# Kernel tuning notes

Hardware: AMD Instinct MI355X
Metric: run time of the kernel (lower is better)

## Reference

```python
import jax, jax.numpy as jnp
import numpy as np
import math

HIDDEN = 2048
HEADS = 16
HEAD_DIM = HIDDEN // HEADS
MAX_SEQ = 4096
ROPE_BASE = 10000.0


def rope_cos_sin(seq_len):
    # (seq_len, head_dim//2) angle table
    inv_freq = 1.0 / (ROPE_BASE ** (jnp.arange(0, HEAD_DIM, 2, dtype=jnp.float32) / HEAD_DIM))
    t = jnp.arange(seq_len, dtype=jnp.float32)
    ang = jnp.einsum('s,f->sf', t, inv_freq)
    return jnp.cos(ang), jnp.sin(ang)


def apply_rope(x, cos, sin):
    # x: (b, s, h, d); interleaved complex pairs along last dim
    b, s, h, d = x.shape
    xr = x.reshape(b, s, h, d // 2, 2)
    x0, x1 = xr[..., 0], xr[..., 1]
    c = cos[:s][None, :, None, :]
    sn = sin[:s][None, :, None, :]
    o0 = x0 * c - x1 * sn
    o1 = x0 * sn + x1 * c
    return jnp.stack([o0, o1], axis=-1).reshape(b, s, h, d)


def setup_inputs() -> dict:
    key = jax.random.key(0)
    k1, k2, k3, k4, k5, k6 = jax.random.split(key, 6)
    B, SQ, SK = 2, 2048, 2048
    x = jax.random.normal(k1, (B, SQ, HIDDEN), dtype=jnp.float32)
    enc = jax.random.normal(k2, (B, SK, HIDDEN), dtype=jnp.float32)
    mask = jnp.ones((B, SK), dtype=jnp.int32)
    scale = 0.02
    Wq = jax.random.normal(k3, (HIDDEN, HIDDEN), dtype=jnp.float32) * scale
    Wk = jax.random.normal(k4, (HIDDEN, HIDDEN), dtype=jnp.float32) * scale
    Wv = jax.random.normal(k5, (HIDDEN, HIDDEN), dtype=jnp.float32) * scale
    Wo = jax.random.normal(k6, (HIDDEN, HIDDEN), dtype=jnp.float32) * scale
    return {"x": x, "encoder_output": enc, "encoder_attention_mask": mask,
            "Wq": Wq, "Wk": Wk, "Wv": Wv, "Wo": Wo}


def reference(x, encoder_output, encoder_attention_mask, Wq, Wk, Wv, Wo):
    B, SQ, _ = x.shape
    SK = encoder_output.shape[1]
    # nn.Linear(bias=False): y = x @ W^T
    q = (x @ Wq.T).reshape(B, SQ, HEADS, HEAD_DIM)
    k = (encoder_output @ Wk.T).reshape(B, SK, HEADS, HEAD_DIM)
    v = (encoder_output @ Wv.T).reshape(B, SK, HEADS, HEAD_DIM)
    cos, sin = rope_cos_sin(max(SQ, SK))
    q = apply_rope(q, cos, sin)
    k = apply_rope(k, cos, sin)
    scale = math.sqrt(HEAD_DIM)
    # (b, h, sq, sk) scores
    scores = jnp.einsum('bqhd,bkhd->bhqk', q, k) / scale
    mask = encoder_attention_mask[:, None, None, :]
    scores = jnp.where(mask == 0, -jnp.inf, scores)
    attn = jax.nn.softmax(scores, axis=-1)
    out = jnp.einsum('bhqk,bkhd->bqhd', attn, v).reshape(B, SQ, HIDDEN)
    return out @ Wo.T
```

## Files before the change

kernel.cpp:

```cpp
#include <hip/hip_runtime.h>
#include <stdint.h>


#define LOG2E 1.44269504088896340736f
#define INV2PI 0.15915494309189535f

typedef __attribute__((ext_vector_type(8))) short bf16x8;
typedef __attribute__((ext_vector_type(8))) uint16_t u16x8;
typedef __attribute__((ext_vector_type(4))) uint16_t u16x4;
typedef __attribute__((ext_vector_type(4))) float f32x4;

__device__ __forceinline__ uint16_t f2bf(float f) {
  union { float f; uint32_t i; } v; v.f = f;
  uint32_t x = v.i;
  return (uint16_t)((x + 0x7fffu + ((x >> 16) & 1u)) >> 16);
}
__device__ __forceinline__ uint32_t f_as_u(float f) { union { float f; uint32_t u; } v; v.f = f; return v.u; }
__device__ __forceinline__ float u_as_f(uint32_t u) { union { uint32_t u; float f; } v; v.u = u; return v.f; }
__device__ __forceinline__ void glds16(const void* g, void* l) {
  __builtin_amdgcn_global_load_lds((const __attribute__((address_space(1))) void*)g,
                                   (__attribute__((address_space(3))) void*)l, 16, 0, 0);
}

__global__ __launch_bounds__(256) void convert_f32_bf16(const float* __restrict__ in,
                                                        uint16_t* __restrict__ out) {
  const long i = ((long)blockIdx.x * 256 + threadIdx.x) * 8;
  const f32x4 a = *(const f32x4*)(in + i);
  const f32x4 b = *(const f32x4*)(in + i + 4);
  u16x8 o;
#pragma unroll
  for (int j = 0; j < 4; ++j) { o[j] = f2bf(a[j]); o[4 + j] = f2bf(b[j]); }
  *(u16x8*)(out + i) = o;
}

__global__ __launch_bounds__(256) void convert_w4(const float* __restrict__ Wq,
                                                  const float* __restrict__ Wk,
                                                  const float* __restrict__ Wv,
                                                  const float* __restrict__ Wo,
                                                  uint16_t* __restrict__ W4) {
  const int blk = blockIdx.x;
  const int sec = blk >> 11;
  const long off = ((long)(blk & 2047) * 256 + threadIdx.x) * 8;
  const float* src = (sec == 0) ? Wq : (sec == 1) ? Wk : (sec == 2) ? Wv : Wo;
  const f32x4 a = *(const f32x4*)(src + off);
  const f32x4 b = *(const f32x4*)(src + off + 4);
  u16x8 o;
#pragma unroll
  for (int j = 0; j < 4; ++j) { o[j] = f2bf(a[j]); o[4 + j] = f2bf(b[j]); }
  *(u16x8*)(W4 + (long)sec * 4194304 + off) = o;
}

__global__ __launch_bounds__(256) void mask_bias(const int* __restrict__ m,
                                                 float* __restrict__ bias) {
  const int i = blockIdx.x * 256 + threadIdx.x;
  bias[i] = m[i] ? 0.0f : -__builtin_inff();
}

#define EPI_QKV 0
#define EPI_F32 1

__device__ __forceinline__ void epi_rope_store(uint16_t* C, const f32x4& a, int rowbase,
                                               int c, float oscale) {
  const int f = (c >> 1) & 63;
  const float inv = __builtin_amdgcn_exp2f((float)f * (-13.287712379549449f / 64.0f));
  const float sgn = (c & 1) ? 1.0f : -1.0f;
#pragma unroll
  for (int r = 0; r < 4; ++r) {
    const float val = a[r];
    const float partner = __shfl_xor(val, 1);
    const int s = (rowbase + r) & 2047;
    const float rev = __builtin_amdgcn_fractf((float)s * inv * INV2PI);
    const float sn = __builtin_amdgcn_sinf(rev);
    const float cs = __builtin_amdgcn_cosf(rev);
    C[(long)(rowbase + r) * 2048 + c] = f2bf((val * cs + sgn * partner * sn) * oscale);
  }
}

template <int MODE>
__global__ __launch_bounds__(256) void gemm_bt(const uint16_t* __restrict__ A0,
                                               const uint16_t* __restrict__ A1,
                                               const uint16_t* __restrict__ W,
                                               void* __restrict__ C0v,
                                               void* __restrict__ C1v,
                                               void* __restrict__ C2v,
                                               int M, int N, int K, float oscale) {
  __shared__ __align__(16) uint16_t As[2][128 * 32];
  __shared__ __align__(16) uint16_t Bs[2][128 * 32];
  const int tid = threadIdx.x;
  const int lane = tid & 63;
  const int w = tid >> 6;
  const int r16 = lane & 15, quad = lane >> 4;
  const int m0 = blockIdx.y * 128, n0 = blockIdx.x * 128;
  const int wm = (w >> 1) * 64, wn = (w & 1) * 64;
  f32x4 acc[4][4] = {};
  const int srow = 32 * w + (lane >> 2);
  const int scol = (lane & 3) * 8;
  const uint16_t* A = (MODE == EPI_QKV && n0 >= 2048) ? A1 : A0;
  const uint16_t* Ag = A + (long)(m0 + srow) * K + scol;
  const uint16_t* Wg = W + (long)(n0 + srow) * K + scol;
  const int co = 2 * w * 512;

  glds16(Ag, &As[0][co]);
  glds16(Ag + (long)16 * K, &As[0][co + 512]);
  glds16(Wg, &Bs[0][co]);
  glds16(Wg + (long)16 * K, &Bs[0][co + 512]);

  auto body = [&](int k1, const uint16_t* Ac, const uint16_t* Bc,
                  uint16_t* An, uint16_t* Bn, bool pf) {
    __syncthreads();
    if (pf) {
      glds16(Ag + k1, An + co);
      glds16(Ag + k1 + (long)16 * K, An + co + 512);
      glds16(Wg + k1, Bn + co);
      glds16(Wg + k1 + (long)16 * K, Bn + co + 512);
    }
    bf16x8 af[4], bfr[4];
#pragma unroll
    for (int mt = 0; mt < 4; ++mt)
      af[mt] = *(const bf16x8*)(Ac + (wm + mt * 16 + r16) * 32 + quad * 8);
#pragma unroll
    for (int nt = 0; nt < 4; ++nt)
      bfr[nt] = *(const bf16x8*)(Bc + (wn + nt * 16 + r16) * 32 + quad * 8);
#pragma unroll
    for (int mt = 0; mt < 4; ++mt)
#pragma unroll
      for (int nt = 0; nt < 4; ++nt)
        acc[mt][nt] = __builtin_amdgcn_mfma_f32_16x16x32_bf16(af[mt], bfr[nt], acc[mt][nt], 0, 0, 0);
  };

  const int NK2 = K >> 6;
  for (int kk = 0; kk < NK2; ++kk) {
    body((2 * kk + 1) * 32, &As[0][0], &Bs[0][0], &As[1][0], &Bs[1][0], true);
    body((2 * kk + 2) * 32, &As[1][0], &Bs[1][0], &As[0][0], &Bs[0][0], kk < NK2 - 1);
  }

#pragma unroll
  for (int mt = 0; mt < 4; ++mt)
#pragma unroll
    for (int nt = 0; nt < 4; ++nt) {
      const int col = n0 + wn + nt * 16 + r16;
      const int rowbase = m0 + wm + mt * 16 + quad * 4;
      if constexpr (MODE == EPI_F32) {
        float* C = (float*)C0v;
#pragma unroll
        for (int r = 0; r < 4; ++r)
          C[(long)(rowbase + r) * N + col] = acc[mt][nt][r];
      } else {
        if (n0 < 2048) {
          epi_rope_store((uint16_t*)C0v, acc[mt][nt], rowbase, col, oscale);
        } else if (n0 < 4096) {
          epi_rope_store((uint16_t*)C1v, acc[mt][nt], rowbase, col - 2048, 1.0f);
        } else {
          uint16_t* Vt = (uint16_t*)C2v;
          const int c = col - 4096;
          const int h = c >> 7, d = c & 127;
          const int b = rowbase >> 11, s = rowbase & 2047;
          u16x4 pk;
#pragma unroll
          for (int r = 0; r < 4; ++r) pk[r] = f2bf(acc[mt][nt][r]);
          *(u16x4*)(Vt + (long)((b * 16 + h) * 128 + d) * 2048 + s) = pk;
        }
      }
    }
}

__global__ __launch_bounds__(256) void attn_kernel(const uint16_t* __restrict__ Q,
                                                   const uint16_t* __restrict__ K,
                                                   const uint16_t* __restrict__ Vt,
                                                   const float* __restrict__ bias,
                                                   uint16_t* __restrict__ O) {
  __shared__ __align__(16) uint16_t Ks[2][32 * 128];
  __shared__ __align__(16) uint16_t Vts[2][128 * 32];
  __shared__ __align__(16) uint16_t Ps[4][32 * 40];
  const int tid = threadIdx.x;
  const int lane = tid & 63;
  const int w = tid >> 6;
  const int r16 = lane & 15, quad = lane >> 4;
  const int h = blockIdx.y, b = blockIdx.z;
  const int qbase = blockIdx.x * 128 + w * 32;

  bf16x8 qf[2][4];
#pragma unroll
  for (int t = 0; t < 2; ++t) {
    const uint16_t* qb = Q + ((long)(b * 2048 + qbase + t * 16 + r16)) * 2048 + h * 128 + quad * 8;
#pragma unroll
    for (int c = 0; c < 4; ++c) qf[t][c] = *(const bf16x8*)(qb + c * 32);
  }
  f32x4 oacc[2][8] = {};
  float li[2][4] = {};

  uint16_t* PsW = &Ps[w][0];
  const float* brow = bias + b * 2048;

  const int key0[2] = {8 * w + quad, 8 * w + 4 + quad};
  const uint16_t* kg[2];
  const uint16_t* vg[2];
#pragma unroll
  for (int i = 0; i < 2; ++i) {
    kg[i] = K + ((long)(b * 2048 + key0[i])) * 2048 + h * 128 + 8 * (r16 ^ ((4 * i + quad) & 7));
    const int dim = 32 * w + 16 * i + (lane >> 2);
    vg[i] = Vt + ((long)((b * 16 + h) * 128 + dim)) * 2048 + 8 * ((lane & 3) ^ ((lane >> 2) & 3));
  }

#pragma unroll
  for (int i = 0; i < 2; ++i) {
    glds16(kg[i], &Ks[0][(2 * w + i) * 512]);
    glds16(vg[i], &Vts[0][(2 * w + i) * 512]);
    kg[i] += 32 * 2048;
    vg[i] += 32;
  }
  float bn0 = brow[r16], bn1 = brow[16 + r16];

  auto body = [&](int k0, const uint16_t* Kc, const uint16_t* Vc,
                  uint16_t* Kn, uint16_t* Vn, bool pf) {
    __syncthreads();
    const float bc0 = bn0, bc1 = bn1;
    if (pf) {
#pragma unroll
      for (int i = 0; i < 2; ++i) {
        glds16(kg[i], Kn + (2 * w + i) * 512);
        glds16(vg[i], Vn + (2 * w + i) * 512);
        kg[i] += 32 * 2048;
        vg[i] += 32;
      }
      bn0 = brow[k0 + 32 + r16];
      bn1 = brow[k0 + 48 + r16];
    }
#pragma unroll
    for (int ct = 0; ct < 2; ++ct) {
      const int key = ct * 16 + r16;
      const int kb = key & 7;
      bf16x8 kf[4];
#pragma unroll
      for (int c = 0; c < 4; ++c)
        kf[c] = *(const bf16x8*)(Kc + key * 128 + ((4 * c + quad) ^ kb) * 8);
      const float bv = ct ? bc1 : bc0;
      const int pc = ct * 2 + (r16 >> 3);
#pragma unroll
      for (int t = 0; t < 2; ++t) {
        f32x4 s = {};
#pragma unroll
        for (int c = 0; c < 4; ++c)
          s = __builtin_amdgcn_mfma_f32_16x16x32_bf16(qf[t][c], kf[c], s, 0, 0, 0);
#pragma unroll
        for (int r = 0; r < 4; ++r) {
          const float p = __builtin_amdgcn_exp2f(s[r] + bv);
          const uint32_t pb = f_as_u(p) + 0x8000u;
          const int row = t * 16 + quad * 4 + r;
          PsW[row * 40 + ((pc ^ r) << 3) + (r16 & 7)] = (uint16_t)(pb >> 16);
          li[t][r] += u_as_f(pb & 0xffff0000u);
        }
      }
    }
    bf16x8 pa[2];
#pragma unroll
    for (int t = 0; t < 2; ++t)
      pa[t] = *(const bf16x8*)(PsW + (t * 16 + r16) * 40 + ((quad ^ (r16 & 3)) << 3));
#pragma unroll
    for (int nt = 0; nt < 8; ++nt) {
      const int dim = nt * 16 + r16;
      bf16x8 vf = *(const bf16x8*)(Vc + dim * 32 + ((quad ^ (dim & 3)) << 3));
#pragma unroll
      for (int t = 0; t < 2; ++t)
        oacc[t][nt] = __builtin_amdgcn_mfma_f32_16x16x32_bf16(pa[t], vf, oacc[t][nt], 0, 0, 0);
    }
  };

  for (int kt2 = 0; kt2 < 32; ++kt2) {
    body(64 * kt2,      &Ks[0][0], &Vts[0][0], &Ks[1][0], &Vts[1][0], true);
    body(64 * kt2 + 32, &Ks[1][0], &Vts[1][0], &Ks[0][0], &Vts[0][0], kt2 < 31);
  }

#pragma unroll
  for (int off = 1; off < 16; off <<= 1)
#pragma unroll
    for (int t = 0; t < 2; ++t)
#pragma unroll
      for (int r = 0; r < 4; ++r) li[t][r] += __shfl_xor(li[t][r], off);

#pragma unroll
  for (int t = 0; t < 2; ++t) {
    uint16_t* ob = O + ((long)(b * 2048 + qbase + t * 16)) * 2048 + h * 128;
    float inv_l[4];
#pragma unroll
    for (int r = 0; r < 4; ++r) inv_l[r] = 1.0f / li[t][r];
#pragma unroll
    for (int nt = 0; nt < 8; ++nt)
#pragma unroll
      for (int r = 0; r < 4; ++r)
        ob[(long)(quad * 4 + r) * 2048 + nt * 16 + r16] = f2bf(oacc[t][nt][r] * inv_l[r]);
  }
}

extern "C" void kernel_launch(void* const* d_in, const int* in_sizes, int n_in,
                              void* d_out, int out_size, void* d_ws, size_t ws_size,
                              hipStream_t stream) {
  const float* x   = (const float*)d_in[0];
  const float* enc = (const float*)d_in[1];
  const int*   msk = (const int*)d_in[2];
  const float* Wq  = (const float*)d_in[3];
  const float* Wk  = (const float*)d_in[4];
  const float* Wv  = (const float*)d_in[5];
  const float* Wo  = (const float*)d_in[6];
  float* out = (float*)d_out;

  const long NELT = 8L * 1024 * 1024;
  const long WELT = 4L * 1024 * 1024;
  uint16_t* Qb  = (uint16_t*)d_ws;
  uint16_t* Kb  = Qb + NELT;
  uint16_t* Vtb = Kb + NELT;
  uint16_t* W4  = Vtb + NELT;
  float* biasb  = (float*)(W4 + 4 * WELT);
  uint16_t* xb   = (uint16_t*)d_out;
  uint16_t* encb = xb + NELT;
  uint16_t* Ob   = W4;

  const float cs_exp = 0.088388347648318447f * LOG2E;

  convert_f32_bf16<<<(int)(NELT / 2048), 256, 0, stream>>>(x, xb);
  convert_f32_bf16<<<(int)(NELT / 2048), 256, 0, stream>>>(enc, encb);
  convert_w4<<<8192, 256, 0, stream>>>(Wq, Wk, Wv, Wo, W4);
  mask_bias<<<16, 256, 0, stream>>>(msk, biasb);

  gemm_bt<EPI_QKV><<<dim3(48, 32), 256, 0, stream>>>(xb, encb, W4, Qb, Kb, Vtb,
                                                     4096, 6144, 2048, cs_exp);

  attn_kernel<<<dim3(16, 16, 2), 256, 0, stream>>>(Qb, Kb, Vtb, biasb, Ob);

  gemm_bt<EPI_F32><<<dim3(16, 32), 256, 0, stream>>>(Ob, nullptr, W4 + 3 * WELT,
                                                     out, nullptr, nullptr,
                                                     4096, 2048, 2048, 1.0f);
}
```

Baseline: 494.1 us.

## Replace 128x128 GEMM with 256x256 tiled, swizzled, pipelined 8-wave kernel

Replaces the 128x128 four-wave GEMM with a 256x256 tile kernel using eight waves, each computing a 128x64 sub-tile. It adds an XOR-swizzled LDS layout to avoid bank conflicts, interleaves global-to-LDS prefetch with MFMA groups under explicit vmcnt waits and barriers, raises priority around the MFMA groups, and remaps workgroup IDs for better L2 locality. The larger tiles give more operand reuse per byte loaded and hide load latency better. The costs are higher register pressure from 32 accumulators per lane and fewer workgroups, only 128 for the output projection, which can leave CUs idle.

```diff
diff --git a/kernel.cpp b/kernel.cpp
--- a/kernel.cpp
+++ b/kernel.cpp
@@ -77,69 +77,101 @@
 }
 
 template <int MODE>
-__global__ __launch_bounds__(256) void gemm_bt(const uint16_t* __restrict__ A0,
-                                               const uint16_t* __restrict__ A1,
-                                               const uint16_t* __restrict__ W,
-                                               void* __restrict__ C0v,
-                                               void* __restrict__ C1v,
-                                               void* __restrict__ C2v,
-                                               int M, int N, int K, float oscale) {
-  __shared__ __align__(16) uint16_t As[2][128 * 32];
-  __shared__ __align__(16) uint16_t Bs[2][128 * 32];
+__global__ __launch_bounds__(512, 2) void gemm256(const uint16_t* __restrict__ A0,
+                                                  const uint16_t* __restrict__ A1,
+                                                  const uint16_t* __restrict__ W,
+                                                  void* __restrict__ C0v,
+                                                  void* __restrict__ C1v,
+                                                  void* __restrict__ C2v,
+                                                  int M, int N, int K, float oscale) {
+  __shared__ __align__(16) uint16_t As[2][2][8192];
+  __shared__ __align__(16) uint16_t Bs[2][2][8192];
   const int tid = threadIdx.x;
   const int lane = tid & 63;
   const int w = tid >> 6;
   const int r16 = lane & 15, quad = lane >> 4;
-  const int m0 = blockIdx.y * 128, n0 = blockIdx.x * 128;
-  const int wm = (w >> 1) * 64, wn = (w & 1) * 64;
-  f32x4 acc[4][4] = {};
-  const int srow = 32 * w + (lane >> 2);
-  const int scol = (lane & 3) * 8;
+  const int wm = w >> 2, wn = w & 3;
+
+  const int nby = M >> 8;
+  const int nwg = gridDim.x;
+  const int wg = ((int)blockIdx.x & 7) * (nwg >> 3) + ((int)blockIdx.x >> 3);
+  const int by = wg % nby, bx = wg / nby;
+  const int m0 = by << 8, n0 = bx << 8;
+
   const uint16_t* A = (MODE == EPI_QKV && n0 >= 2048) ? A1 : A0;
-  const uint16_t* Ag = A + (long)(m0 + srow) * K + scol;
-  const uint16_t* Wg = W + (long)(n0 + srow) * K + scol;
-  const int co = 2 * w * 512;
-
-  glds16(Ag, &As[0][co]);
-  glds16(Ag + (long)16 * K, &As[0][co + 512]);
-  glds16(Wg, &Bs[0][co]);
-  glds16(Wg + (long)16 * K, &Bs[0][co + 512]);
-
-  auto body = [&](int k1, const uint16_t* Ac, const uint16_t* Bc,
-                  uint16_t* An, uint16_t* Bn, bool pf) {
-    __syncthreads();
-    if (pf) {
-      glds16(Ag + k1, An + co);
-      glds16(Ag + k1 + (long)16 * K, An + co + 512);
-      glds16(Wg + k1, Bn + co);
-      glds16(Wg + k1 + (long)16 * K, Bn + co + 512);
-    }
-    bf16x8 af[4], bfr[4];
-#pragma unroll
-    for (int mt = 0; mt < 4; ++mt)
-      af[mt] = *(const bf16x8*)(Ac + (wm + mt * 16 + r16) * 32 + quad * 8);
-#pragma unroll
-    for (int nt = 0; nt < 4; ++nt)
-      bfr[nt] = *(const bf16x8*)(Bc + (wn + nt * 16 + r16) * 32 + quad * 8);
-#pragma unroll
-    for (int mt = 0; mt < 4; ++mt)
-#pragma unroll
-      for (int nt = 0; nt < 4; ++nt)
-        acc[mt][nt] = __builtin_amdgcn_mfma_f32_16x16x32_bf16(af[mt], bfr[nt], acc[mt][nt], 0, 0, 0);
-  };
-
-  const int NK2 = K >> 6;
-  for (int kk = 0; kk < NK2; ++kk) {
-    body((2 * kk + 1) * 32, &As[0][0], &Bs[0][0], &As[1][0], &Bs[1][0], true);
-    body((2 * kk + 2) * 32, &As[1][0], &Bs[1][0], &As[0][0], &Bs[0][0], kk < NK2 - 1);
-  }
-
-#pragma unroll
-  for (int mt = 0; mt < 4; ++mt)
+
+  const int srow = 2 * w * 16 + (lane >> 2);
+  const int ssl = (lane & 3) ^ ((srow >> 1) & 3);
+  const uint16_t* Ag0 = A + (long)(m0 + srow) * K + ssl * 8;
+  const uint16_t* Ag1 = Ag0 + (long)16 * K;
+  const uint16_t* Bg0 = W + (long)(n0 + srow) * K + ssl * 8;
+  const uint16_t* Bg1 = Bg0 + (long)16 * K;
+  const int ldso = w << 10;
+
+  const int sw = (r16 >> 1) & 3;
+  const int aoff = (wm * 128 + r16) * 32 + ((quad ^ sw) << 3);
+  const int boff = (wn * 64 + r16) * 32 + ((quad ^ sw) << 3);
+
+  f32x4 acc[8][4] = {};
+  bf16x8 af[4], bfr[4];
+
+#define SCHED0() __builtin_amdgcn_sched_barrier(0)
+#define G_STAGE_A(BUF, KK, T) do { \
+    glds16(Ag0 + (long)(T) * 64 + (KK) * 32, &As[BUF][KK][ldso]); \
+    glds16(Ag1 + (long)(T) * 64 + (KK) * 32, &As[BUF][KK][ldso + 512]); } while (0)
+#define G_STAGE_B(BUF, KK, T) do { \
+    glds16(Bg0 + (long)(T) * 64 + (KK) * 32, &Bs[BUF][KK][ldso]); \
+    glds16(Bg1 + (long)(T) * 64 + (KK) * 32, &Bs[BUF][KK][ldso + 512]); } while (0)
+#define LDS_B(BUF, KK) do { _Pragma("unroll") \
+    for (int i = 0; i < 4; ++i) bfr[i] = *(const bf16x8*)&Bs[BUF][KK][boff + i * 512]; } while (0)
+#define LDS_A(BUF, KK, MH) do { _Pragma("unroll") \
+    for (int i = 0; i < 4; ++i) af[i] = *(const bf16x8*)&As[BUF][KK][aoff + ((MH) * 4 + i) * 512]; } while (0)
+#define MFMA16(MH) do { __builtin_amdgcn_s_setprio(1); _Pragma("unroll") \
+    for (int mi = 0; mi < 4; ++mi) { _Pragma("unroll") \
+      for (int nt = 0; nt < 4; ++nt) \
+        acc[(MH) * 4 + mi][nt] = __builtin_amdgcn_mfma_f32_16x16x32_bf16(af[mi], bfr[nt], acc[(MH) * 4 + mi][nt], 0, 0, 0); } \
+    __builtin_amdgcn_s_setprio(0); } while (0)
+#define VMBAR(NN) do { SCHED0(); \
+    asm volatile("s_waitcnt vmcnt(" #NN ")" ::: "memory"); \
+    __builtin_amdgcn_s_barrier(); \
+    SCHED0(); } while (0)
+#define TILE_ITER(T, BC, BN) do { \
+    G_STAGE_A(BN, 0, (T) + 1); LDS_B(BC, 0); LDS_A(BC, 0, 0); MFMA16(0); \
+    G_STAGE_B(BN, 0, (T) + 1); LDS_A(BC, 0, 1); MFMA16(1); \
+    VMBAR(4); \
+    G_STAGE_A(BN, 1, (T) + 1); LDS_B(BC, 1); LDS_A(BC, 1, 0); MFMA16(0); \
+    G_STAGE_B(BN, 1, (T) + 1); LDS_A(BC, 1, 1); MFMA16(1); \
+    VMBAR(4); } while (0)
+
+  G_STAGE_A(0, 0, 0); G_STAGE_B(0, 0, 0); G_STAGE_A(0, 1, 0); G_STAGE_B(0, 1, 0);
+  VMBAR(4);
+
+  const int NT = K >> 6;
+  int t = 0;
+  for (; t + 2 < NT; t += 2) { TILE_ITER(t, 0, 1); TILE_ITER(t + 1, 1, 0); }
+  TILE_ITER(t, 0, 1);
+
+  LDS_B(1, 0); LDS_A(1, 0, 0); MFMA16(0);
+  LDS_A(1, 0, 1); MFMA16(1);
+  VMBAR(0);
+  LDS_B(1, 1); LDS_A(1, 1, 0); MFMA16(0);
+  LDS_A(1, 1, 1); MFMA16(1);
+
+#undef SCHED0
+#undef G_STAGE_A
+#undef G_STAGE_B
+#undef LDS_A
+#undef LDS_B
+#undef MFMA16
+#undef VMBAR
+#undef TILE_ITER
+
+#pragma unroll
+  for (int mt = 0; mt < 8; ++mt)
 #pragma unroll
     for (int nt = 0; nt < 4; ++nt) {
-      const int col = n0 + wn + nt * 16 + r16;
-      const int rowbase = m0 + wm + mt * 16 + quad * 4;
+      const int col = n0 + wn * 64 + nt * 16 + r16;
+      const int rowbase = m0 + wm * 128 + mt * 16 + quad * 4;
       if constexpr (MODE == EPI_F32) {
         float* C = (float*)C0v;
 #pragma unroll
@@ -322,12 +354,12 @@
   convert_w4<<<8192, 256, 0, stream>>>(Wq, Wk, Wv, Wo, W4);
   mask_bias<<<16, 256, 0, stream>>>(msk, biasb);
 
-  gemm_bt<EPI_QKV><<<dim3(48, 32), 256, 0, stream>>>(xb, encb, W4, Qb, Kb, Vtb,
-                                                     4096, 6144, 2048, cs_exp);
+  gemm256<EPI_QKV><<<384, 512, 0, stream>>>(xb, encb, W4, Qb, Kb, Vtb,
+                                            4096, 6144, 2048, cs_exp);
 
   attn_kernel<<<dim3(16, 16, 2), 256, 0, stream>>>(Qb, Kb, Vtb, biasb, Ob);
 
-  gemm_bt<EPI_F32><<<dim3(16, 32), 256, 0, stream>>>(Ob, nullptr, W4 + 3 * WELT,
-                                                     out, nullptr, nullptr,
-                                                     4096, 2048, 2048, 1.0f);
-}
+  gemm256<EPI_F32><<<128, 512, 0, stream>>>(Ob, nullptr, W4 + 3 * WELT,
+                                            out, nullptr, nullptr,
+                                            4096, 2048, 2048, 1.0f);
+}
```

Result: faster. 461.2 us (-6.7%).
